# Kernel optimization log

Hardware: AMD Instinct MI355X
Metric: run time of the kernel (lower is better)

Reference implementation:

```python
import jax, jax.numpy as jnp
import numpy as np

B, R, A, V, L = 256, 512, 196, 10000, 2
I = R  # input_size == rnn_size (required for stacked layers)


def setup_inputs() -> dict:
    key = jax.random.key(0)
    ks = jax.random.split(key, 18)
    s = 0.05
    return {
        "x": jax.random.normal(ks[0], (B, I), jnp.float32),
        "att": jax.random.normal(ks[1], (B, A, R), jnp.float32),
        "inputs": jax.random.normal(ks[2], (2 * L, B, R), jnp.float32),
        "Wa2a": jax.random.normal(ks[3], (A, R), jnp.float32) * s,
        "ba2a": jnp.zeros((A,), jnp.float32),
        "Wh2a": jax.random.normal(ks[4], (A, R), jnp.float32) * s,
        "bh2a": jnp.zeros((A,), jnp.float32),
        "wd2d": jax.random.normal(ks[5], (A,), jnp.float32) * s,
        "bd2d": jnp.zeros((1,), jnp.float32),
        "Wi2h": jax.random.normal(ks[6], (4 * R, I), jnp.float32) * s,
        "bi2h": jnp.zeros((4 * R,), jnp.float32),
        "Wh2h": jax.random.normal(ks[7], (4 * R, R), jnp.float32) * s,
        "bh2h": jnp.zeros((4 * R,), jnp.float32),
        "Wr2a": jax.random.normal(ks[8], (4 * R, R), jnp.float32) * s,
        "br2a": jnp.zeros((4 * R,), jnp.float32),
        "Wproj": jax.random.normal(ks[9], (V, R), jnp.float32) * s,
        "bproj": jnp.zeros((V,), jnp.float32),
    }


def reference(x, att, inputs, Wa2a, ba2a, Wh2a, bh2a, wd2d, bd2d,
              Wi2h, bi2h, Wh2h, bh2h, Wr2a, br2a, Wproj, bproj):
    # att: [B, A, R]  (A spatial positions, R features); inputs: [2L, B, R]
    states = []
    cur = x
    # a2a(att) is layer-independent but the original recomputes it; einsum below
    # is cheap so we keep the per-layer structure faithful & simple.
    for i in range(L):
        prev_c = inputs[2 * i]
        prev_h = inputs[2 * i + 1]
        # attention scoring: att_v[b,i,a] + att_h[b,i] (unsqueeze(2).expand)
        att_v = jnp.einsum('bir,ar->bia', att, Wa2a) + ba2a          # [B,A,A]
        att_h = prev_h @ Wh2a.T + bh2a                               # [B,A]
        dot = jnp.tanh(att_v + att_h[:, :, None])                    # [B,A,A]
        score = jnp.einsum('bia,a->bi', dot, wd2d) + bd2d            # [B,A]
        w = jax.nn.softmax(score, axis=-1)                           # [B,A]
        att_res = jnp.einsum('bir,bi->br', att, w)                   # [B,R]
        sums = (cur @ Wi2h.T + bi2h) + (prev_h @ Wh2h.T + bh2h) + (att_res @ Wr2a.T + br2a)
        gates = jax.nn.sigmoid(sums[:, :3 * R])
        in_gate = gates[:, :R]
        forget_gate = gates[:, R:2 * R]
        out_gate = gates[:, 2 * R:3 * R]
        in_transform = jnp.tanh(sums[:, 3 * R:])
        next_c = forget_gate * prev_c + in_gate * in_transform
        next_h = out_gate * jnp.tanh(next_c)
        states.append(next_c)
        states.append(next_h)
        cur = next_h
    logsoft = jax.nn.log_softmax(cur @ Wproj.T + bproj, axis=-1)     # [B,V]
    return jnp.stack(states), logsoft
```

## Files before the change

### kernel.cpp

```cpp
#include <hip/hip_runtime.h>
#include <hip/hip_bf16.h>
#include <cstdint>
#include <cstddef>

#define BB 256
#define RR 512
#define AA 196
#define VV 10000
#define MATT (BB*AA)
#define NT13 13

typedef float f32x4 __attribute__((ext_vector_type(4)));
typedef __bf16 bf16x8 __attribute__((ext_vector_type(8)));
typedef __bf16 bf16x4 __attribute__((ext_vector_type(4)));

#define MFMA16(a,b,c) __builtin_amdgcn_mfma_f32_16x16x32_bf16(a,b,c,0,0,0)

__device__ __forceinline__ float fast_tanh(float x){
  float ax = fabsf(x);
  float e = __expf(-2.0f*ax);
  float t = __fdividef(1.0f - e, 1.0f + e);
  return x < 0.0f ? -t : t;
}

__device__ __forceinline__ void gload16(const void* gsrc, void* ldsdst){
  __builtin_amdgcn_global_load_lds(
      (const __attribute__((address_space(1))) unsigned int*)gsrc,
      (__attribute__((address_space(3))) unsigned int*)ldsdst,
      16, 0, 0);
}

#define ABAR   asm volatile("s_barrier" ::: "memory")
#define WVM(N) asm volatile("s_waitcnt vmcnt(" #N ")" ::: "memory")

#define CVT8(a, f0, f1) do { \
  a[0]=(__bf16)(f0).x; a[1]=(__bf16)(f0).y; a[2]=(__bf16)(f0).z; a[3]=(__bf16)(f0).w; \
  a[4]=(__bf16)(f1).x; a[5]=(__bf16)(f1).y; a[6]=(__bf16)(f1).z; a[7]=(__bf16)(f1).w; \
} while(0)

__global__ void cvt4_k(const float* __restrict__ src, __bf16* __restrict__ dst, int n4){
  int i = blockIdx.x*256 + threadIdx.x;
  if (i < n4){
    float4 v = ((const float4*)src)[i];
    bf16x4 o;
    o[0]=(__bf16)v.x; o[1]=(__bf16)v.y; o[2]=(__bf16)v.z; o[3]=(__bf16)v.w;
    ((bf16x4*)dst)[i] = o;
  }
}

__global__ void cvt_padrows_k(const float* __restrict__ src, __bf16* __restrict__ dst, int nvalid){
  int i = blockIdx.x*256 + threadIdx.x;
  int row = i >> 9;
  dst[i] = (__bf16)((row < nvalid) ? src[(size_t)row*512 + (i & 511)] : 0.0f);
}

__global__ void wcat2_k(const float* __restrict__ Wi2h, const float* __restrict__ Wh2h,
                        const float* __restrict__ Wr2a, __bf16* __restrict__ Wcat){
  int k = blockIdx.x*256 + threadIdx.x;
  int n = blockIdx.y;
  float v;
  if (k < 512)       v = Wi2h[n*512 + k];
  else if (k < 1024) v = Wh2h[n*512 + (k-512)];
  else               v = Wr2a[n*512 + (k-1024)];
  Wcat[(size_t)n*1536 + k] = (__bf16)v;
}

__global__ void build_small_k(const float* __restrict__ ba2a, const float* __restrict__ wd2d,
                              const float* __restrict__ bi2h, const float* __restrict__ bh2h,
                              const float* __restrict__ br2a,
                              float* __restrict__ ba_pad, float* __restrict__ wd_pad,
                              float* __restrict__ bcat){
  int i = blockIdx.x*256 + threadIdx.x;
  if (i < 2048){
    bcat[i] = bi2h[i] + bh2h[i] + br2a[i];
  } else if (i < 2048+208){
    int j = i - 2048; ba_pad[j] = (j < AA) ? ba2a[j] : 0.0f;
  } else if (i < 2048+416){
    int j = i - 2256; wd_pad[j] = (j < AA) ? wd2d[j] : 0.0f;
  }
}

__global__ __launch_bounds__(256,4) void gemm3_k(
    const __bf16* __restrict__ A, const __bf16* __restrict__ Bw,
    const float* __restrict__ bias, float* __restrict__ C,
    int N, int K, int NC)
{
  __shared__ __bf16 AshAll[3*2048];
  __shared__ __bf16 BshAll[3*4096];
  const int t = threadIdx.x;
  const int l = t & 63;
  const int w = t >> 6;
  const int l15 = l & 15;
  const int g  = l >> 4;
  const int rho = l15 & 7;
  const int mrow = blockIdx.y*32;
  const int ncb  = blockIdx.x*64;

  const int arow = t >> 3, aj = t & 7;
  const __bf16* as_ = A + (size_t)(mrow + arow)*K + ((aj ^ (arow&7)) << 3);
  const int aoff = w*512;
  const __bf16* bs0_ = Bw + (size_t)(ncb + arow)*K      + ((aj ^ (arow&7)) << 3);
  const __bf16* bs1_ = Bw + (size_t)(ncb + 32 + arow)*K + ((aj ^ (arow&7)) << 3);
  const int boff0 = w*512;
  const int boff1 = 2048 + w*512;

#define G3_STAGE(B, CH) do { \
    gload16(as_  + (CH)*64, AshAll + (B)*2048 + aoff); \
    gload16(bs0_ + (CH)*64, BshAll + (B)*4096 + boff0); \
    gload16(bs1_ + (CH)*64, BshAll + (B)*4096 + boff1); \
  } while(0)

  f32x4 acc0 = {}, acc1 = {};

#define G3_COMPUTE(B) do { \
    const __bf16* As_ = AshAll + (B)*2048; \
    const __bf16* Bs_ = BshAll + (B)*4096; \
    _Pragma("unroll") \
    for (int s_ = 0; s_ < 2; s_++){ \
      int q_ = (((s_<<2)+g) ^ rho) << 3; \
      bf16x8 a0_ = *(const bf16x8*)(As_ + l15*64 + q_); \
      bf16x8 a1_ = *(const bf16x8*)(As_ + (l15+16)*64 + q_); \
      bf16x8 b_  = *(const bf16x8*)(Bs_ + (w*16+l15)*64 + q_); \
      acc0 = MFMA16(a0_, b_, acc0); \
      acc1 = MFMA16(a1_, b_, acc1); \
    } \
  } while(0)

  G3_STAGE(0,0); G3_STAGE(1,1); G3_STAGE(2,2);
  WVM(6); ABAR;
  int buf = 0;
  for (int c = 0; c < NC; c++){
    G3_COMPUTE(buf);
    if (c + 3 < NC){
      ABAR;
      G3_STAGE(buf, c+3);
      WVM(6); ABAR;
    } else if (c == NC-3){
      WVM(3); ABAR;
    } else if (c == NC-2){
      WVM(0); ABAR;
    }
    buf = (buf == 2) ? 0 : buf + 1;
  }

  int col = ncb + w*16 + l15;
  if (col < N){
    float bv = bias[col];
    #pragma unroll
    for (int r = 0; r < 4; r++){
      C[(size_t)(mrow + g*4 + r)*N + col]      = acc0[r] + bv;
      C[(size_t)(mrow + 16 + g*4 + r)*N + col] = acc1[r] + bv;
    }
  }
#undef G3_STAGE
#undef G3_COMPUTE
}

__global__ __launch_bounds__(256,2) void att_score5_k(
    const float* __restrict__ att, const __bf16* __restrict__ Wa2a_p,
    const float* __restrict__ ba_pad, const float* __restrict__ wd_pad,
    const float* __restrict__ att_h, float* __restrict__ score)
{
  __shared__ __bf16 Bsh[3*13312];
  const int t = threadIdx.x;
  const int l = t & 63;
  const int w = t >> 6;
  const int l15 = l & 15;
  const int g  = l >> 4;
  const int rho = l15 & 7;
  const int rowbase = blockIdx.x * 64;

  const __bf16* bsrc[7]; int bslot[7];
  #pragma unroll
  for (int i = 0; i < 7; i++){
    int id = i*4 + w;
    if (id >= 26) id -= 2;
    int slotbase = id*64;
    int slot = slotbase + l;
    int row = slot >> 3;
    int j   = slot & 7;
    bslot[i] = slotbase*8;
    bsrc[i]  = Wa2a_p + (size_t)row*RR + ((j ^ (row&7))<<3);
  }

  const float* pa = att + (size_t)(rowbase + w*16 + l15)*RR + g*8;

  f32x4 acc[NT13] = {};
  float4 p00,p01,p02,p03, p10,p11,p12,p13, p20,p21,p22,p23;

#define SC_STAGE(B, KC) do { \
    _Pragma("unroll") \
    for (int i_ = 0; i_ < 7; i_++) gload16(bsrc[i_] + (KC), Bsh + (B)*13312 + bslot[i_]); \
  } while(0)
#define SC_LOADA(S, KC) do { \
    p##S##0 = *(const float4*)(pa + (KC)); \
    p##S##1 = *(const float4*)(pa + (KC) + 4); \
    p##S##2 = *(const float4*)(pa + (KC) + 32); \
    p##S##3 = *(const float4*)(pa + (KC) + 36); \
  } while(0)
#define SC_COMPUTE(B, S) do { \
    { bf16x8 a_; CVT8(a_, p##S##0, p##S##1); \
      const int sw_ = (g ^ rho) << 3; \
      _Pragma("unroll") \
      for (int nt_ = 0; nt_ < NT13; nt_++){ \
        bf16x8 b_ = *(const bf16x8*)&Bsh[(B)*13312 + nt_*1024 + l15*64 + sw_]; \
        acc[nt_] = MFMA16(a_, b_, acc[nt_]); } } \
    { bf16x8 a_; CVT8(a_, p##S##2, p##S##3); \
      const int sw_ = ((4 + g) ^ rho) << 3; \
      _Pragma("unroll") \
      for (int nt_ = 0; nt_ < NT13; nt_++){ \
        bf16x8 b_ = *(const bf16x8*)&Bsh[(B)*13312 + nt_*1024 + l15*64 + sw_]; \
        acc[nt_] = MFMA16(a_, b_, acc[nt_]); } } \
  } while(0)

  SC_STAGE(0,0);   SC_LOADA(0,0);
  SC_STAGE(1,64);  SC_LOADA(1,64);
  SC_STAGE(2,128); SC_LOADA(2,128);
  WVM(22); ABAR;
  SC_COMPUTE(0,0); ABAR; SC_STAGE(0,192); SC_LOADA(0,192); WVM(22); ABAR;
  SC_COMPUTE(1,1); ABAR; SC_STAGE(1,256); SC_LOADA(1,256); WVM(22); ABAR;
  SC_COMPUTE(2,2); ABAR; SC_STAGE(2,320); SC_LOADA(2,320); WVM(22); ABAR;
  SC_COMPUTE(0,0); ABAR; SC_STAGE(0,384); SC_LOADA(0,384); WVM(22); ABAR;
  SC_COMPUTE(1,1); ABAR; SC_STAGE(1,448); SC_LOADA(1,448); WVM(22); ABAR;
  SC_COMPUTE(2,2); WVM(11); ABAR;
  SC_COMPUTE(0,0); WVM(0);  ABAR;
  SC_COMPUTE(1,1);

  float wdv[NT13], bav[NT13];
  #pragma unroll
  for (int nt = 0; nt < NT13; nt++){
    int col = nt*16 + l15;
    wdv[nt] = wd_pad[col];
    bav[nt] = ba_pad[col];
  }
  #pragma unroll
  for (int r = 0; r < 4; r++){
    int row = rowbase + w*16 + g*4 + r;
    float ah0 = att_h[row];
    float ah1 = att_h[MATT + row];
    float s0 = 0.0f, s1 = 0.0f;
    #pragma unroll
    for (int nt = 0; nt < NT13; nt++){
      float v = acc[nt][r] + bav[nt];
      s0 += fast_tanh(v + ah0) * wdv[nt];
      s1 += fast_tanh(v + ah1) * wdv[nt];
    }
    #pragma unroll
    for (int o = 1; o < 16; o <<= 1){
      s0 += __shfl_xor(s0, o, 16);
      s1 += __shfl_xor(s1, o, 16);
    }
    if (l15 == 0){
      score[row] = s0;
      score[MATT + row] = s1;
    }
  }
#undef SC_STAGE
#undef SC_LOADA
#undef SC_COMPUTE
}

__global__ void softmax196_k(const float* __restrict__ score, float* __restrict__ wsm){
  int lb = blockIdx.x;
  int t = threadIdx.x;
  const float* s = score + (size_t)lb*AA;
  float v0 = (t      < AA) ? s[t]       : -3.4e38f;
  float v1 = (t+64   < AA) ? s[t+64]    : -3.4e38f;
  float v2 = (t+128  < AA) ? s[t+128]   : -3.4e38f;
  float v3 = (t+192  < AA) ? s[t+192]   : -3.4e38f;
  float mx = fmaxf(fmaxf(v0,v1), fmaxf(v2,v3));
  #pragma unroll
  for (int o = 1; o < 64; o <<= 1) mx = fmaxf(mx, __shfl_xor(mx, o, 64));
  float e0 = (t      < AA) ? __expf(v0 - mx) : 0.0f;
  float e1 = (t+64   < AA) ? __expf(v1 - mx) : 0.0f;
  float e2 = (t+128  < AA) ? __expf(v2 - mx) : 0.0f;
  float e3 = (t+192  < AA) ? __expf(v3 - mx) : 0.0f;
  float sum = e0+e1+e2+e3;
  #pragma unroll
  for (int o = 1; o < 64; o <<= 1) sum += __shfl_xor(sum, o, 64);
  float inv = 1.0f / sum;
  float* o_ = wsm + (size_t)lb*AA;
  if (t      < AA) o_[t]     = e0*inv;
  if (t+64   < AA) o_[t+64]  = e1*inv;
  if (t+128  < AA) o_[t+128] = e2*inv;
  if (t+192  < AA) o_[t+192] = e3*inv;
}

__global__ __launch_bounds__(512) void attres3_k(
    const float* __restrict__ att, const float* __restrict__ wsm,
    const float* __restrict__ x, const float* __restrict__ inputs,
    __bf16* __restrict__ Xcat0, __bf16* __restrict__ Xcat1){
  int b = blockIdx.x, t = threadIdx.x;
  __shared__ float w0[208], w1[208];
  __shared__ float4 redv[4][128];
  if (t < AA) w0[t] = wsm[(size_t)b*AA + t];
  int t2 = t - 256;
  if (t2 >= 0 && t2 < AA) w1[t2] = wsm[(size_t)(256+b)*AA + t2];
  Xcat0[(size_t)b*1536 + t]       = (__bf16)x[(size_t)b*512 + t];
  Xcat0[(size_t)b*1536 + 512 + t] = (__bf16)inputs[(size_t)1*131072 + b*512 + t];
  Xcat1[(size_t)b*1536 + 512 + t] = (__bf16)inputs[(size_t)3*131072 + b*512 + t];
  __syncthreads();
  int cg = t & 127, ig = t >> 7;
  const float4* ap = (const float4*)(att + (size_t)b*AA*RR) + cg;
  float4 s0 = {0,0,0,0}, s1 = {0,0,0,0};
  #pragma unroll 4
  for (int i = ig; i < AA; i += 4){
    float4 v = ap[(size_t)i*128];
    float a0 = w0[i], a1 = w1[i];
    s0.x += v.x*a0; s0.y += v.y*a0; s0.z += v.z*a0; s0.w += v.w*a0;
    s1.x += v.x*a1; s1.y += v.y*a1; s1.z += v.z*a1; s1.w += v.w*a1;
  }
  redv[ig][cg] = s0; __syncthreads();
  if (t < 128){
    float4 a = redv[0][t], b4 = redv[1][t], c4 = redv[2][t], d4 = redv[3][t];
    __bf16* o = Xcat0 + (size_t)b*1536 + 1024 + t*4;
    o[0]=(__bf16)(a.x+b4.x+c4.x+d4.x); o[1]=(__bf16)(a.y+b4.y+c4.y+d4.y);
    o[2]=(__bf16)(a.z+b4.z+c4.z+d4.z); o[3]=(__bf16)(a.w+b4.w+c4.w+d4.w);
  }
  __syncthreads();
  redv[ig][cg] = s1; __syncthreads();
  if (t < 128){
    float4 a = redv[0][t], b4 = redv[1][t], c4 = redv[2][t], d4 = redv[3][t];
    __bf16* o = Xcat1 + (size_t)b*1536 + 1024 + t*4;
    o[0]=(__bf16)(a.x+b4.x+c4.x+d4.x); o[1]=(__bf16)(a.y+b4.y+c4.y+d4.y);
    o[2]=(__bf16)(a.z+b4.z+c4.z+d4.z); o[3]=(__bf16)(a.w+b4.w+c4.w+d4.w);
  }
}

__global__ void gate_k(const float* __restrict__ sums, const float* __restrict__ prev_c,
                       float* __restrict__ out_c, float* __restrict__ out_h,
                       __bf16* __restrict__ hdst, int hstride){
  int idx = blockIdx.x*256 + threadIdx.x;
  int b = idx >> 9, r = idx & 511;
  const float* s = sums + (size_t)b*2048;
  float ig = 1.0f/(1.0f + __expf(-s[r]));
  float fg = 1.0f/(1.0f + __expf(-s[512+r]));
  float og = 1.0f/(1.0f + __expf(-s[1024+r]));
  float g  = fast_tanh(s[1536+r]);
  float c = fg*prev_c[idx] + ig*g;
  float h = og*fast_tanh(c);
  out_c[idx] = c;
  out_h[idx] = h;
  hdst[(size_t)b*hstride + r] = (__bf16)h;
}

__global__ void logsoftmax_k(const float* __restrict__ logits, float* __restrict__ out){
  int b = blockIdx.x, t = threadIdx.x;
  __shared__ float red[4], red2[4];
  const float* p = logits + (size_t)b*VV;
  float mx = -3.4e38f;
  for (int i = t; i < VV; i += 256) mx = fmaxf(mx, p[i]);
  #pragma unroll
  for (int o = 1; o < 64; o <<= 1) mx = fmaxf(mx, __shfl_xor(mx, o, 64));
  if ((t & 63) == 0) red[t >> 6] = mx;
  __syncthreads();
  mx = fmaxf(fmaxf(red[0], red[1]), fmaxf(red[2], red[3]));
  float sum = 0.0f;
  for (int i = t; i < VV; i += 256) sum += __expf(p[i] - mx);
  #pragma unroll
  for (int o = 1; o < 64; o <<= 1) sum += __shfl_xor(sum, o, 64);
  if ((t & 63) == 0) red2[t >> 6] = sum;
  __syncthreads();
  sum = red2[0] + red2[1] + red2[2] + red2[3];
  float lse = mx + logf(sum);
  float* q = out + (size_t)b*VV;
  for (int i = t; i < VV; i += 256) q[i] = p[i] - lse;
}

extern "C" void kernel_launch(void* const* d_in, const int* in_sizes, int n_in,
                              void* d_out_, int out_size, void* d_ws, size_t ws_size,
                              hipStream_t stream){
  const float* x     = (const float*)d_in[0];
  const float* att   = (const float*)d_in[1];
  const float* inputs= (const float*)d_in[2];
  const float* Wa2a  = (const float*)d_in[3];
  const float* ba2a  = (const float*)d_in[4];
  const float* Wh2a  = (const float*)d_in[5];
  const float* bh2a  = (const float*)d_in[6];
  const float* wd2d  = (const float*)d_in[7];
  const float* Wi2h  = (const float*)d_in[9];
  const float* bi2h  = (const float*)d_in[10];
  const float* Wh2h  = (const float*)d_in[11];
  const float* bh2h  = (const float*)d_in[12];
  const float* Wr2a  = (const float*)d_in[13];
  const float* br2a  = (const float*)d_in[14];
  const float* Wproj = (const float*)d_in[15];
  const float* bproj = (const float*)d_in[16];
  float* d_out = (float*)d_out_;

  char* wsp = (char*)d_ws;
  auto alloc = [&](size_t bytes)->char*{
    char* p = wsp;
    wsp += (bytes + 255) & ~(size_t)255;
    return p;
  };
  __bf16* Wa2a_p   = (__bf16*)alloc((size_t)208*RR*2);
  __bf16* Wh2a_pad = (__bf16*)alloc((size_t)256*RR*2);
  __bf16* Wcat_bf  = (__bf16*)alloc((size_t)2048*1536*2);
  __bf16* Wproj_bf = (__bf16*)alloc((size_t)10048*RR*2);
  __bf16* inp_bf   = (__bf16*)alloc((size_t)512*RR*2);
  float* ba_pad = (float*)alloc(208*4);
  float* wd_pad = (float*)alloc(208*4);
  float* bcat   = (float*)alloc(2048*4);
  float* att_h  = (float*)alloc((size_t)2*MATT*4);
  float* score  = (float*)alloc((size_t)2*MATT*4);
  float* wsm    = (float*)alloc((size_t)2*MATT*4);
  __bf16* Xcat0 = (__bf16*)alloc((size_t)BB*1536*2);
  __bf16* Xcat1 = (__bf16*)alloc((size_t)BB*1536*2);
  float* sums   = (float*)alloc((size_t)BB*2048*4);
  __bf16* h1_bf = (__bf16*)alloc((size_t)BB*RR*2);
  float* logits = (float*)alloc((size_t)BB*VV*4);

  cvt_padrows_k<<<(208*512)/256, 256, 0, stream>>>(Wa2a, Wa2a_p, AA);
  cvt_padrows_k<<<(256*512)/256, 256, 0, stream>>>(Wh2a, Wh2a_pad, AA);
  cvt_padrows_k<<<(10048*512)/256, 256, 0, stream>>>(Wproj, Wproj_bf, VV);
  cvt4_k<<<(131072/4)/256, 256, 0, stream>>>(inputs + 1*131072, inp_bf, 131072/4);
  cvt4_k<<<(131072/4)/256, 256, 0, stream>>>(inputs + 3*131072, inp_bf + 131072, 131072/4);
  wcat2_k<<<dim3(6,2048), 256, 0, stream>>>(Wi2h, Wh2h, Wr2a, Wcat_bf);
  build_small_k<<<10, 256, 0, stream>>>(ba2a, wd2d, bi2h, bh2h, br2a, ba_pad, wd_pad, bcat);

  gemm3_k<<<dim3(4,16), 256, 0, stream>>>(inp_bf, Wh2a_pad, bh2a, att_h, AA, 512, 8);
  att_score5_k<<<784, 256, 0, stream>>>(att, Wa2a_p, ba_pad, wd_pad, att_h, score);
  softmax196_k<<<512, 64, 0, stream>>>(score, wsm);
  attres3_k<<<256, 512, 0, stream>>>(att, wsm, x, inputs, Xcat0, Xcat1);

  gemm3_k<<<dim3(32,8), 256, 0, stream>>>(Xcat0, Wcat_bf, bcat, sums, 2048, 1536, 24);
  gate_k<<<512, 256, 0, stream>>>(sums, inputs, d_out, d_out + 131072, Xcat1, 1536);
  gemm3_k<<<dim3(32,8), 256, 0, stream>>>(Xcat1, Wcat_bf, bcat, sums, 2048, 1536, 24);
  gate_k<<<512, 256, 0, stream>>>(sums, inputs + 2*131072, d_out + 2*131072, d_out + 3*131072, h1_bf, 512);

  gemm3_k<<<dim3(157,8), 256, 0, stream>>>(h1_bf, Wproj_bf, bproj, logits, VV, 512, 8);
  logsoftmax_k<<<256, 256, 0, stream>>>(logits, d_out + 4*131072);
}
```

Baseline: 166.5 us.

## Pre-convert att to bf16 and retile attention scoring with split N halves

Adds a pass that converts the full att tensor to bf16 once. The attention-score kernel is restructured to stage both att and Wa2a tiles into LDS via async loads, using 128-row by 128-column tiles over a 2D grid, and writes partial scores per column half. The softmax then sums the two halves, and the att-weighted reduction reads the bf16 att copy. The intent is to reduce per-block register and LDS pressure, raise occupancy and halve att read traffic in later kernels. The cost is an extra conversion pass over about 100 MB of fp32 att, plus padding the A dimension to 256, which does wasted MFMA work on the padded columns.

```diff
diff --git a/kernel.cpp b/kernel.cpp
--- a/kernel.cpp
+++ b/kernel.cpp
@@ -8,7 +8,7 @@
 #define AA 196
 #define VV 10000
 #define MATT (BB*AA)
-#define NT13 13
+#define NT8 8
 
 typedef float f32x4 __attribute__((ext_vector_type(4)));
 typedef __bf16 bf16x8 __attribute__((ext_vector_type(8)));
@@ -32,11 +32,6 @@
 
 #define ABAR   asm volatile("s_barrier" ::: "memory")
 #define WVM(N) asm volatile("s_waitcnt vmcnt(" #N ")" ::: "memory")
-
-#define CVT8(a, f0, f1) do { \
-  a[0]=(__bf16)(f0).x; a[1]=(__bf16)(f0).y; a[2]=(__bf16)(f0).z; a[3]=(__bf16)(f0).w; \
-  a[4]=(__bf16)(f1).x; a[5]=(__bf16)(f1).y; a[6]=(__bf16)(f1).z; a[7]=(__bf16)(f1).w; \
-} while(0)
 
 __global__ void cvt4_k(const float* __restrict__ src, __bf16* __restrict__ dst, int n4){
   int i = blockIdx.x*256 + threadIdx.x;
@@ -73,10 +68,10 @@
   int i = blockIdx.x*256 + threadIdx.x;
   if (i < 2048){
     bcat[i] = bi2h[i] + bh2h[i] + br2a[i];
-  } else if (i < 2048+208){
+  } else if (i < 2048+256){
     int j = i - 2048; ba_pad[j] = (j < AA) ? ba2a[j] : 0.0f;
-  } else if (i < 2048+416){
-    int j = i - 2256; wd_pad[j] = (j < AA) ? wd2d[j] : 0.0f;
+  } else if (i < 2048+512){
+    int j = i - 2304; wd_pad[j] = (j < AA) ? wd2d[j] : 0.0f;
   }
 }
 
@@ -156,118 +151,121 @@
 #undef G3_COMPUTE
 }
 
-__global__ __launch_bounds__(256,2) void att_score5_k(
-    const float* __restrict__ att, const __bf16* __restrict__ Wa2a_p,
+__global__ __launch_bounds__(256,3) void att_score6_k(
+    const __bf16* __restrict__ att_bf, const __bf16* __restrict__ Wa2a_p,
     const float* __restrict__ ba_pad, const float* __restrict__ wd_pad,
-    const float* __restrict__ att_h, float* __restrict__ score)
+    const float* __restrict__ att_h, float* __restrict__ sp)
 {
-  __shared__ __bf16 Bsh[3*13312];
+  __shared__ __bf16 Ash[3*4096];
+  __shared__ __bf16 Bsh[3*4096];
   const int t = threadIdx.x;
   const int l = t & 63;
   const int w = t >> 6;
   const int l15 = l & 15;
   const int g  = l >> 4;
-  const int rho = l15 & 7;
-  const int rowbase = blockIdx.x * 64;
-
-  const __bf16* bsrc[7]; int bslot[7];
-  #pragma unroll
-  for (int i = 0; i < 7; i++){
+  const int rowbase = blockIdx.x * 128;
+  const int half = blockIdx.y;
+
+  const __bf16* asrc[2]; const __bf16* bsrc[2]; int slotb[2];
+  #pragma unroll
+  for (int i = 0; i < 2; i++){
     int id = i*4 + w;
-    if (id >= 26) id -= 2;
-    int slotbase = id*64;
-    int slot = slotbase + l;
-    int row = slot >> 3;
-    int j   = slot & 7;
-    bslot[i] = slotbase*8;
-    bsrc[i]  = Wa2a_p + (size_t)row*RR + ((j ^ (row&7))<<3);
-  }
-
-  const float* pa = att + (size_t)(rowbase + w*16 + l15)*RR + g*8;
-
-  f32x4 acc[NT13] = {};
-  float4 p00,p01,p02,p03, p10,p11,p12,p13, p20,p21,p22,p23;
-
-#define SC_STAGE(B, KC) do { \
+    int slot = id*64 + l;
+    int row = slot >> 2, j = slot & 3;
+    int jj = j ^ ((row>>1)&3);
+    slotb[i] = id*512;
+    asrc[i] = att_bf + (size_t)(rowbase + row)*RR + (jj<<3);
+    bsrc[i] = Wa2a_p + (size_t)(half*128 + row)*RR + (jj<<3);
+  }
+
+  f32x4 acc0[NT8] = {}; f32x4 acc1[NT8] = {};
+
+#define S6_STAGE(BC, KC) do { \
+    gload16(asrc[0] + (KC), Ash + (BC)*4096 + slotb[0]); \
+    gload16(asrc[1] + (KC), Ash + (BC)*4096 + slotb[1]); \
+    gload16(bsrc[0] + (KC), Bsh + (BC)*4096 + slotb[0]); \
+    gload16(bsrc[1] + (KC), Bsh + (BC)*4096 + slotb[1]); \
+  } while(0)
+
+  const int r0 = w*32 + l15, r1 = r0 + 16;
+  const int ao0 = r0*32 + ((g ^ ((r0>>1)&3))<<3);
+  const int ao1 = r1*32 + ((g ^ ((r1>>1)&3))<<3);
+
+#define S6_COMPUTE(BC) do { \
+    const __bf16* As_ = Ash + (BC)*4096; \
+    const __bf16* Bs_ = Bsh + (BC)*4096; \
+    bf16x8 a0_ = *(const bf16x8*)(As_ + ao0); \
+    bf16x8 a1_ = *(const bf16x8*)(As_ + ao1); \
     _Pragma("unroll") \
-    for (int i_ = 0; i_ < 7; i_++) gload16(bsrc[i_] + (KC), Bsh + (B)*13312 + bslot[i_]); \
+    for (int nt_ = 0; nt_ < NT8; nt_++){ \
+      int br_ = nt_*16 + l15; \
+      bf16x8 b_ = *(const bf16x8*)(Bs_ + br_*32 + ((g ^ ((br_>>1)&3))<<3)); \
+      acc0[nt_] = MFMA16(a0_, b_, acc0[nt_]); \
+      acc1[nt_] = MFMA16(a1_, b_, acc1[nt_]); \
+    } \
   } while(0)
-#define SC_LOADA(S, KC) do { \
-    p##S##0 = *(const float4*)(pa + (KC)); \
-    p##S##1 = *(const float4*)(pa + (KC) + 4); \
-    p##S##2 = *(const float4*)(pa + (KC) + 32); \
-    p##S##3 = *(const float4*)(pa + (KC) + 36); \
-  } while(0)
-#define SC_COMPUTE(B, S) do { \
-    { bf16x8 a_; CVT8(a_, p##S##0, p##S##1); \
-      const int sw_ = (g ^ rho) << 3; \
-      _Pragma("unroll") \
-      for (int nt_ = 0; nt_ < NT13; nt_++){ \
-        bf16x8 b_ = *(const bf16x8*)&Bsh[(B)*13312 + nt_*1024 + l15*64 + sw_]; \
-        acc[nt_] = MFMA16(a_, b_, acc[nt_]); } } \
-    { bf16x8 a_; CVT8(a_, p##S##2, p##S##3); \
-      const int sw_ = ((4 + g) ^ rho) << 3; \
-      _Pragma("unroll") \
-      for (int nt_ = 0; nt_ < NT13; nt_++){ \
-        bf16x8 b_ = *(const bf16x8*)&Bsh[(B)*13312 + nt_*1024 + l15*64 + sw_]; \
-        acc[nt_] = MFMA16(a_, b_, acc[nt_]); } } \
-  } while(0)
-
-  SC_STAGE(0,0);   SC_LOADA(0,0);
-  SC_STAGE(1,64);  SC_LOADA(1,64);
-  SC_STAGE(2,128); SC_LOADA(2,128);
-  WVM(22); ABAR;
-  SC_COMPUTE(0,0); ABAR; SC_STAGE(0,192); SC_LOADA(0,192); WVM(22); ABAR;
-  SC_COMPUTE(1,1); ABAR; SC_STAGE(1,256); SC_LOADA(1,256); WVM(22); ABAR;
-  SC_COMPUTE(2,2); ABAR; SC_STAGE(2,320); SC_LOADA(2,320); WVM(22); ABAR;
-  SC_COMPUTE(0,0); ABAR; SC_STAGE(0,384); SC_LOADA(0,384); WVM(22); ABAR;
-  SC_COMPUTE(1,1); ABAR; SC_STAGE(1,448); SC_LOADA(1,448); WVM(22); ABAR;
-  SC_COMPUTE(2,2); WVM(11); ABAR;
-  SC_COMPUTE(0,0); WVM(0);  ABAR;
-  SC_COMPUTE(1,1);
-
-  float wdv[NT13], bav[NT13];
-  #pragma unroll
-  for (int nt = 0; nt < NT13; nt++){
-    int col = nt*16 + l15;
+
+  S6_STAGE(0,0); S6_STAGE(1,32); S6_STAGE(2,64);
+  WVM(8); ABAR;
+  #pragma unroll
+  for (int c = 0; c < 16; c++){
+    S6_COMPUTE(c%3);
+    if (c < 13){
+      ABAR;
+      S6_STAGE(c%3, (c+3)*32);
+      WVM(8); ABAR;
+    } else if (c == 13){
+      WVM(4); ABAR;
+    } else if (c == 14){
+      WVM(0); ABAR;
+    }
+  }
+
+  float wdv[NT8], bav[NT8];
+  #pragma unroll
+  for (int nt = 0; nt < NT8; nt++){
+    int col = half*128 + nt*16 + l15;
     wdv[nt] = wd_pad[col];
     bav[nt] = ba_pad[col];
   }
   #pragma unroll
-  for (int r = 0; r < 4; r++){
-    int row = rowbase + w*16 + g*4 + r;
-    float ah0 = att_h[row];
-    float ah1 = att_h[MATT + row];
-    float s0 = 0.0f, s1 = 0.0f;
+  for (int mt = 0; mt < 2; mt++){
     #pragma unroll
-    for (int nt = 0; nt < NT13; nt++){
-      float v = acc[nt][r] + bav[nt];
-      s0 += fast_tanh(v + ah0) * wdv[nt];
-      s1 += fast_tanh(v + ah1) * wdv[nt];
+    for (int r = 0; r < 4; r++){
+      int row = rowbase + w*32 + mt*16 + g*4 + r;
+      float ah0 = att_h[row];
+      float ah1 = att_h[MATT + row];
+      float s0 = 0.0f, s1 = 0.0f;
+      #pragma unroll
+      for (int nt = 0; nt < NT8; nt++){
+        float v = (mt ? acc1[nt][r] : acc0[nt][r]) + bav[nt];
+        s0 += fast_tanh(v + ah0) * wdv[nt];
+        s1 += fast_tanh(v + ah1) * wdv[nt];
+      }
+      #pragma unroll
+      for (int o = 1; o < 16; o <<= 1){
+        s0 += __shfl_xor(s0, o, 16);
+        s1 += __shfl_xor(s1, o, 16);
+      }
+      if (l15 == 0){
+        sp[(size_t)half*2*MATT + row]        = s0;
+        sp[(size_t)half*2*MATT + MATT + row] = s1;
+      }
     }
-    #pragma unroll
-    for (int o = 1; o < 16; o <<= 1){
-      s0 += __shfl_xor(s0, o, 16);
-      s1 += __shfl_xor(s1, o, 16);
-    }
-    if (l15 == 0){
-      score[row] = s0;
-      score[MATT + row] = s1;
-    }
-  }
-#undef SC_STAGE
-#undef SC_LOADA
-#undef SC_COMPUTE
-}
-
-__global__ void softmax196_k(const float* __restrict__ score, float* __restrict__ wsm){
+  }
+#undef S6_STAGE
+#undef S6_COMPUTE
+}
+
+__global__ void softmax196b_k(const float* __restrict__ sp, float* __restrict__ wsm){
   int lb = blockIdx.x;
   int t = threadIdx.x;
-  const float* s = score + (size_t)lb*AA;
-  float v0 = (t      < AA) ? s[t]       : -3.4e38f;
-  float v1 = (t+64   < AA) ? s[t+64]    : -3.4e38f;
-  float v2 = (t+128  < AA) ? s[t+128]   : -3.4e38f;
-  float v3 = (t+192  < AA) ? s[t+192]   : -3.4e38f;
+  const float* p = sp + (size_t)(lb>>8)*MATT + (size_t)(lb&255)*AA;
+  const float* q = p + (size_t)2*MATT;
+  float v0 = (t      < AA) ? p[t]     + q[t]     : -3.4e38f;
+  float v1 = (t+64   < AA) ? p[t+64]  + q[t+64]  : -3.4e38f;
+  float v2 = (t+128  < AA) ? p[t+128] + q[t+128] : -3.4e38f;
+  float v3 = (t+192  < AA) ? p[t+192] + q[t+192] : -3.4e38f;
   float mx = fmaxf(fmaxf(v0,v1), fmaxf(v2,v3));
   #pragma unroll
   for (int o = 1; o < 64; o <<= 1) mx = fmaxf(mx, __shfl_xor(mx, o, 64));
@@ -286,13 +284,13 @@
   if (t+192  < AA) o_[t+192] = e3*inv;
 }
 
-__global__ __launch_bounds__(512) void attres3_k(
-    const float* __restrict__ att, const float* __restrict__ wsm,
+__global__ __launch_bounds__(512) void attres4_k(
+    const __bf16* __restrict__ att_bf, const float* __restrict__ wsm,
     const float* __restrict__ x, const float* __restrict__ inputs,
     __bf16* __restrict__ Xcat0, __bf16* __restrict__ Xcat1){
   int b = blockIdx.x, t = threadIdx.x;
-  __shared__ float w0[208], w1[208];
-  __shared__ float4 redv[4][128];
+  __shared__ float w0[AA+4], w1[AA+4];
+  __shared__ float red[8][520];
   if (t < AA) w0[t] = wsm[(size_t)b*AA + t];
   int t2 = t - 256;
   if (t2 >= 0 && t2 < AA) w1[t2] = wsm[(size_t)(256+b)*AA + t2];
@@ -300,30 +298,36 @@
   Xcat0[(size_t)b*1536 + 512 + t] = (__bf16)inputs[(size_t)1*131072 + b*512 + t];
   Xcat1[(size_t)b*1536 + 512 + t] = (__bf16)inputs[(size_t)3*131072 + b*512 + t];
   __syncthreads();
-  int cg = t & 127, ig = t >> 7;
-  const float4* ap = (const float4*)(att + (size_t)b*AA*RR) + cg;
-  float4 s0 = {0,0,0,0}, s1 = {0,0,0,0};
-  #pragma unroll 4
-  for (int i = ig; i < AA; i += 4){
-    float4 v = ap[(size_t)i*128];
+  int cg = t & 63, ig = t >> 6;
+  const __bf16* ap = att_bf + (size_t)b*AA*RR + cg*8;
+  float s0[8] = {}, s1[8] = {};
+  for (int i = ig; i < AA; i += 8){
+    bf16x8 v = *(const bf16x8*)(ap + (size_t)i*RR);
     float a0 = w0[i], a1 = w1[i];
-    s0.x += v.x*a0; s0.y += v.y*a0; s0.z += v.z*a0; s0.w += v.w*a0;
-    s1.x += v.x*a1; s1.y += v.y*a1; s1.z += v.z*a1; s1.w += v.w*a1;
-  }
-  redv[ig][cg] = s0; __syncthreads();
-  if (t < 128){
-    float4 a = redv[0][t], b4 = redv[1][t], c4 = redv[2][t], d4 = redv[3][t];
-    __bf16* o = Xcat0 + (size_t)b*1536 + 1024 + t*4;
-    o[0]=(__bf16)(a.x+b4.x+c4.x+d4.x); o[1]=(__bf16)(a.y+b4.y+c4.y+d4.y);
-    o[2]=(__bf16)(a.z+b4.z+c4.z+d4.z); o[3]=(__bf16)(a.w+b4.w+c4.w+d4.w);
-  }
-  __syncthreads();
-  redv[ig][cg] = s1; __syncthreads();
-  if (t < 128){
-    float4 a = redv[0][t], b4 = redv[1][t], c4 = redv[2][t], d4 = redv[3][t];
-    __bf16* o = Xcat1 + (size_t)b*1536 + 1024 + t*4;
-    o[0]=(__bf16)(a.x+b4.x+c4.x+d4.x); o[1]=(__bf16)(a.y+b4.y+c4.y+d4.y);
-    o[2]=(__bf16)(a.z+b4.z+c4.z+d4.z); o[3]=(__bf16)(a.w+b4.w+c4.w+d4.w);
+    #pragma unroll
+    for (int e = 0; e < 8; e++){
+      float f = (float)v[e];
+      s0[e] += f*a0; s1[e] += f*a1;
+    }
+  }
+  #pragma unroll
+  for (int e = 0; e < 8; e++) red[ig][cg*8+e] = s0[e];
+  __syncthreads();
+  {
+    float a = 0;
+    #pragma unroll
+    for (int q = 0; q < 8; q++) a += red[q][t];
+    Xcat0[(size_t)b*1536 + 1024 + t] = (__bf16)a;
+  }
+  __syncthreads();
+  #pragma unroll
+  for (int e = 0; e < 8; e++) red[ig][cg*8+e] = s1[e];
+  __syncthreads();
+  {
+    float a = 0;
+    #pragma unroll
+    for (int q = 0; q < 8; q++) a += red[q][t];
+    Xcat1[(size_t)b*1536 + 1024 + t] = (__bf16)a;
   }
 }
 
@@ -394,16 +398,17 @@
     wsp += (bytes + 255) & ~(size_t)255;
     return p;
   };
-  __bf16* Wa2a_p   = (__bf16*)alloc((size_t)208*RR*2);
+  __bf16* att_bf   = (__bf16*)alloc((size_t)MATT*RR*2);
+  __bf16* Wa2a_p   = (__bf16*)alloc((size_t)256*RR*2);
   __bf16* Wh2a_pad = (__bf16*)alloc((size_t)256*RR*2);
   __bf16* Wcat_bf  = (__bf16*)alloc((size_t)2048*1536*2);
   __bf16* Wproj_bf = (__bf16*)alloc((size_t)10048*RR*2);
   __bf16* inp_bf   = (__bf16*)alloc((size_t)512*RR*2);
-  float* ba_pad = (float*)alloc(208*4);
-  float* wd_pad = (float*)alloc(208*4);
+  float* ba_pad = (float*)alloc(256*4);
+  float* wd_pad = (float*)alloc(256*4);
   float* bcat   = (float*)alloc(2048*4);
   float* att_h  = (float*)alloc((size_t)2*MATT*4);
-  float* score  = (float*)alloc((size_t)2*MATT*4);
+  float* sp     = (float*)alloc((size_t)4*MATT*4);
   float* wsm    = (float*)alloc((size_t)2*MATT*4);
   __bf16* Xcat0 = (__bf16*)alloc((size_t)BB*1536*2);
   __bf16* Xcat1 = (__bf16*)alloc((size_t)BB*1536*2);
@@ -411,7 +416,8 @@
   __bf16* h1_bf = (__bf16*)alloc((size_t)BB*RR*2);
   float* logits = (float*)alloc((size_t)BB*VV*4);
 
-  cvt_padrows_k<<<(208*512)/256, 256, 0, stream>>>(Wa2a, Wa2a_p, AA);
+  cvt4_k<<<(MATT*RR/4)/256, 256, 0, stream>>>(att, att_bf, MATT*RR/4);
+  cvt_padrows_k<<<(256*512)/256, 256, 0, stream>>>(Wa2a, Wa2a_p, AA);
   cvt_padrows_k<<<(256*512)/256, 256, 0, stream>>>(Wh2a, Wh2a_pad, AA);
   cvt_padrows_k<<<(10048*512)/256, 256, 0, stream>>>(Wproj, Wproj_bf, VV);
   cvt4_k<<<(131072/4)/256, 256, 0, stream>>>(inputs + 1*131072, inp_bf, 131072/4);
@@ -420,9 +426,9 @@
   build_small_k<<<10, 256, 0, stream>>>(ba2a, wd2d, bi2h, bh2h, br2a, ba_pad, wd_pad, bcat);
 
   gemm3_k<<<dim3(4,16), 256, 0, stream>>>(inp_bf, Wh2a_pad, bh2a, att_h, AA, 512, 8);
-  att_score5_k<<<784, 256, 0, stream>>>(att, Wa2a_p, ba_pad, wd_pad, att_h, score);
-  softmax196_k<<<512, 64, 0, stream>>>(score, wsm);
-  attres3_k<<<256, 512, 0, stream>>>(att, wsm, x, inputs, Xcat0, Xcat1);
+  att_score6_k<<<dim3(392,2), 256, 0, stream>>>(att_bf, Wa2a_p, ba_pad, wd_pad, att_h, sp);
+  softmax196b_k<<<512, 64, 0, stream>>>(sp, wsm);
+  attres4_k<<<256, 512, 0, stream>>>(att_bf, wsm, x, inputs, Xcat0, Xcat1);
 
   gemm3_k<<<dim3(32,8), 256, 0, stream>>>(Xcat0, Wcat_bf, bcat, sums, 2048, 1536, 24);
   gate_k<<<512, 256, 0, stream>>>(sums, inputs, d_out, d_out + 131072, Xcat1, 1536);
```

New measurement: 181.5 us. 9.0% more time.

## Fuse attention scoring, softmax and weighted sum into one per-batch kernel

Applied to the files above, without the earlier changes.

Replaces the three kernels for attention scoring (MFMA GEMM plus tanh dot), softmax and attention-weighted sum with a single kernel that runs one block per batch row. Each block computes its 196x196 (padded to 256) score tile through LDS double-buffering, reduces and softmaxes in shared memory, then re-reads att for the weighted sum. This removes the score and softmax-weight global round trips and two launches. In exchange the grid drops to 256 blocks, padding wastes MFMA work, and att is read twice within the block (the second read may hit cache).

```diff
diff --git a/kernel.cpp b/kernel.cpp
--- a/kernel.cpp
+++ b/kernel.cpp
@@ -8,7 +8,6 @@
 #define AA 196
 #define VV 10000
 #define MATT (BB*AA)
-#define NT13 13
 
 typedef float f32x4 __attribute__((ext_vector_type(4)));
 typedef __bf16 bf16x8 __attribute__((ext_vector_type(8)));
@@ -73,10 +72,10 @@
   int i = blockIdx.x*256 + threadIdx.x;
   if (i < 2048){
     bcat[i] = bi2h[i] + bh2h[i] + br2a[i];
-  } else if (i < 2048+208){
+  } else if (i < 2048+256){
     int j = i - 2048; ba_pad[j] = (j < AA) ? ba2a[j] : 0.0f;
-  } else if (i < 2048+416){
-    int j = i - 2256; wd_pad[j] = (j < AA) ? wd2d[j] : 0.0f;
+  } else if (i < 2048+512){
+    int j = i - 2304; wd_pad[j] = (j < AA) ? wd2d[j] : 0.0f;
   }
 }
 
@@ -156,175 +155,183 @@
 #undef G3_COMPUTE
 }
 
-__global__ __launch_bounds__(256,2) void att_score5_k(
+__global__ __launch_bounds__(512,2) void attfull_k(
     const float* __restrict__ att, const __bf16* __restrict__ Wa2a_p,
     const float* __restrict__ ba_pad, const float* __restrict__ wd_pad,
-    const float* __restrict__ att_h, float* __restrict__ score)
+    const float* __restrict__ att_h, const float* __restrict__ x,
+    const float* __restrict__ inputs,
+    __bf16* __restrict__ Xcat0, __bf16* __restrict__ Xcat1)
 {
-  __shared__ __bf16 Bsh[3*13312];
+  __shared__ char smem[67584];
   const int t = threadIdx.x;
+  const int b = blockIdx.x;
   const int l = t & 63;
   const int w = t >> 6;
-  const int l15 = l & 15;
-  const int g  = l >> 4;
-  const int rho = l15 & 7;
-  const int rowbase = blockIdx.x * 64;
-
-  const __bf16* bsrc[7]; int bslot[7];
-  #pragma unroll
-  for (int i = 0; i < 7; i++){
-    int id = i*4 + w;
-    if (id >= 26) id -= 2;
-    int slotbase = id*64;
-    int slot = slotbase + l;
-    int row = slot >> 3;
-    int j   = slot & 7;
-    bslot[i] = slotbase*8;
-    bsrc[i]  = Wa2a_p + (size_t)row*RR + ((j ^ (row&7))<<3);
-  }
-
-  const float* pa = att + (size_t)(rowbase + w*16 + l15)*RR + g*8;
-
-  f32x4 acc[NT13] = {};
-  float4 p00,p01,p02,p03, p10,p11,p12,p13, p20,p21,p22,p23;
-
-#define SC_STAGE(B, KC) do { \
-    _Pragma("unroll") \
-    for (int i_ = 0; i_ < 7; i_++) gload16(bsrc[i_] + (KC), Bsh + (B)*13312 + bslot[i_]); \
-  } while(0)
-#define SC_LOADA(S, KC) do { \
-    p##S##0 = *(const float4*)(pa + (KC)); \
-    p##S##1 = *(const float4*)(pa + (KC) + 4); \
-    p##S##2 = *(const float4*)(pa + (KC) + 32); \
-    p##S##3 = *(const float4*)(pa + (KC) + 36); \
-  } while(0)
-#define SC_COMPUTE(B, S) do { \
-    { bf16x8 a_; CVT8(a_, p##S##0, p##S##1); \
-      const int sw_ = (g ^ rho) << 3; \
-      _Pragma("unroll") \
-      for (int nt_ = 0; nt_ < NT13; nt_++){ \
-        bf16x8 b_ = *(const bf16x8*)&Bsh[(B)*13312 + nt_*1024 + l15*64 + sw_]; \
-        acc[nt_] = MFMA16(a_, b_, acc[nt_]); } } \
-    { bf16x8 a_; CVT8(a_, p##S##2, p##S##3); \
-      const int sw_ = ((4 + g) ^ rho) << 3; \
-      _Pragma("unroll") \
-      for (int nt_ = 0; nt_ < NT13; nt_++){ \
-        bf16x8 b_ = *(const bf16x8*)&Bsh[(B)*13312 + nt_*1024 + l15*64 + sw_]; \
-        acc[nt_] = MFMA16(a_, b_, acc[nt_]); } } \
-  } while(0)
-
-  SC_STAGE(0,0);   SC_LOADA(0,0);
-  SC_STAGE(1,64);  SC_LOADA(1,64);
-  SC_STAGE(2,128); SC_LOADA(2,128);
-  WVM(22); ABAR;
-  SC_COMPUTE(0,0); ABAR; SC_STAGE(0,192); SC_LOADA(0,192); WVM(22); ABAR;
-  SC_COMPUTE(1,1); ABAR; SC_STAGE(1,256); SC_LOADA(1,256); WVM(22); ABAR;
-  SC_COMPUTE(2,2); ABAR; SC_STAGE(2,320); SC_LOADA(2,320); WVM(22); ABAR;
-  SC_COMPUTE(0,0); ABAR; SC_STAGE(0,384); SC_LOADA(0,384); WVM(22); ABAR;
-  SC_COMPUTE(1,1); ABAR; SC_STAGE(1,448); SC_LOADA(1,448); WVM(22); ABAR;
-  SC_COMPUTE(2,2); WVM(11); ABAR;
-  SC_COMPUTE(0,0); WVM(0);  ABAR;
-  SC_COMPUTE(1,1);
-
-  float wdv[NT13], bav[NT13];
-  #pragma unroll
-  for (int nt = 0; nt < NT13; nt++){
-    int col = nt*16 + l15;
-    wdv[nt] = wd_pad[col];
-    bav[nt] = ba_pad[col];
-  }
-  #pragma unroll
-  for (int r = 0; r < 4; r++){
-    int row = rowbase + w*16 + g*4 + r;
-    float ah0 = att_h[row];
-    float ah1 = att_h[MATT + row];
-    float s0 = 0.0f, s1 = 0.0f;
-    #pragma unroll
-    for (int nt = 0; nt < NT13; nt++){
-      float v = acc[nt][r] + bav[nt];
-      s0 += fast_tanh(v + ah0) * wdv[nt];
-      s1 += fast_tanh(v + ah1) * wdv[nt];
-    }
-    #pragma unroll
-    for (int o = 1; o < 16; o <<= 1){
-      s0 += __shfl_xor(s0, o, 16);
-      s1 += __shfl_xor(s1, o, 16);
-    }
-    if (l15 == 0){
-      score[row] = s0;
-      score[MATT + row] = s1;
-    }
-  }
-#undef SC_STAGE
-#undef SC_LOADA
-#undef SC_COMPUTE
-}
-
-__global__ void softmax196_k(const float* __restrict__ score, float* __restrict__ wsm){
-  int lb = blockIdx.x;
-  int t = threadIdx.x;
-  const float* s = score + (size_t)lb*AA;
-  float v0 = (t      < AA) ? s[t]       : -3.4e38f;
-  float v1 = (t+64   < AA) ? s[t+64]    : -3.4e38f;
-  float v2 = (t+128  < AA) ? s[t+128]   : -3.4e38f;
-  float v3 = (t+192  < AA) ? s[t+192]   : -3.4e38f;
-  float mx = fmaxf(fmaxf(v0,v1), fmaxf(v2,v3));
-  #pragma unroll
-  for (int o = 1; o < 64; o <<= 1) mx = fmaxf(mx, __shfl_xor(mx, o, 64));
-  float e0 = (t      < AA) ? __expf(v0 - mx) : 0.0f;
-  float e1 = (t+64   < AA) ? __expf(v1 - mx) : 0.0f;
-  float e2 = (t+128  < AA) ? __expf(v2 - mx) : 0.0f;
-  float e3 = (t+192  < AA) ? __expf(v3 - mx) : 0.0f;
-  float sum = e0+e1+e2+e3;
-  #pragma unroll
-  for (int o = 1; o < 64; o <<= 1) sum += __shfl_xor(sum, o, 64);
-  float inv = 1.0f / sum;
-  float* o_ = wsm + (size_t)lb*AA;
-  if (t      < AA) o_[t]     = e0*inv;
-  if (t+64   < AA) o_[t+64]  = e1*inv;
-  if (t+128  < AA) o_[t+128] = e2*inv;
-  if (t+192  < AA) o_[t+192] = e3*inv;
-}
-
-__global__ __launch_bounds__(512) void attres3_k(
-    const float* __restrict__ att, const float* __restrict__ wsm,
-    const float* __restrict__ x, const float* __restrict__ inputs,
-    __bf16* __restrict__ Xcat0, __bf16* __restrict__ Xcat1){
-  int b = blockIdx.x, t = threadIdx.x;
-  __shared__ float w0[208], w1[208];
-  __shared__ float4 redv[4][128];
-  if (t < AA) w0[t] = wsm[(size_t)b*AA + t];
-  int t2 = t - 256;
-  if (t2 >= 0 && t2 < AA) w1[t2] = wsm[(size_t)(256+b)*AA + t2];
+  const int wr = w >> 2, wc = w & 3;
+  const int l15 = l & 15, g = l >> 4;
+
   Xcat0[(size_t)b*1536 + t]       = (__bf16)x[(size_t)b*512 + t];
   Xcat0[(size_t)b*1536 + 512 + t] = (__bf16)inputs[(size_t)1*131072 + b*512 + t];
   Xcat1[(size_t)b*1536 + 512 + t] = (__bf16)inputs[(size_t)3*131072 + b*512 + t];
-  __syncthreads();
-  int cg = t & 127, ig = t >> 7;
-  const float4* ap = (const float4*)(att + (size_t)b*AA*RR) + cg;
+  float* ahsh = (float*)(smem + 65536);
+  { int li = t >> 8, i = t & 255;
+    ahsh[li*256 + i] = (i < AA) ? att_h[((size_t)li*256 + b)*AA + i] : 0.0f; }
+
+  const int sr = t >> 1, sh = t & 1;
+  const float*  aSrc = att + ((size_t)b*AA + (sr < AA ? sr : AA-1))*RR + sh*16;
+  const __bf16* bSrc = Wa2a_p + (size_t)sr*RR + sh*16;
+  const int rb = sr*64;
+  const int q0 = (((sh*2)   ^ (sr&3))<<4);
+  const int q1 = (((sh*2+1) ^ (sr&3))<<4);
+
+  f32x4 acc[8][4] = {};
+  float4 af0, af1, af2, af3;
+  uint4  bq0, bq1;
+
+  const int aswz  = (g ^ (l15&3)) << 4;
+  const int abase = (wr*128 + l15)*64 + aswz;
+  const int bbase = (wc*64  + l15)*64 + aswz;
+
+#define AF_LOADP(KC) do { \
+    af0 = *(const float4*)(aSrc + (KC));      af1 = *(const float4*)(aSrc + (KC) + 4); \
+    af2 = *(const float4*)(aSrc + (KC) + 8);  af3 = *(const float4*)(aSrc + (KC) + 12); \
+    bq0 = *(const uint4*)(bSrc + (KC));       bq1 = *(const uint4*)(bSrc + (KC) + 8); \
+  } while(0)
+
+#define STAGE_WR(BUF) do { \
+    char* Ab = smem + (BUF)*16384; \
+    char* Bb = smem + 32768 + (BUF)*16384; \
+    bf16x8 w0_, w1_; CVT8(w0_, af0, af1); CVT8(w1_, af2, af3); \
+    *(bf16x8*)(Ab + rb + q0) = w0_; \
+    *(bf16x8*)(Ab + rb + q1) = w1_; \
+    *(uint4*)(Bb + rb + q0) = bq0; \
+    *(uint4*)(Bb + rb + q1) = bq1; \
+  } while(0)
+
+#define K_COMPUTE(BUF) do { \
+    const char* Ab = smem + (BUF)*16384; \
+    const char* Bb = smem + 32768 + (BUF)*16384; \
+    bf16x8 bfr[4]; \
+    _Pragma("unroll") \
+    for (int ct = 0; ct < 4; ct++) bfr[ct] = *(const bf16x8*)(Bb + bbase + ct*1024); \
+    _Pragma("unroll") \
+    for (int rt = 0; rt < 8; rt++){ \
+      bf16x8 afr = *(const bf16x8*)(Ab + abase + rt*1024); \
+      _Pragma("unroll") \
+      for (int ct = 0; ct < 4; ct++) acc[rt][ct] = MFMA16(afr, bfr[ct], acc[rt][ct]); \
+    } \
+  } while(0)
+
+  AF_LOADP(0);
+  STAGE_WR(0);
+  AF_LOADP(32);
+  __syncthreads();
+  #pragma unroll
+  for (int c = 0; c < 16; c++){
+    K_COMPUTE(c & 1);
+    if (c < 15) STAGE_WR((c+1) & 1);
+    if (c < 14) AF_LOADP((c+2)*32);
+    __syncthreads();
+  }
+
+  float bav[4], wdv[4];
+  #pragma unroll
+  for (int ct = 0; ct < 4; ct++){
+    int col = wc*64 + ct*16 + l15;
+    bav[ct] = ba_pad[col];
+    wdv[ct] = wd_pad[col];
+  }
+  float* spart = (float*)smem;
+  #pragma unroll
+  for (int rt = 0; rt < 8; rt++){
+    #pragma unroll
+    for (int rg = 0; rg < 4; rg++){
+      int row = wr*128 + rt*16 + g*4 + rg;
+      float ah0 = ahsh[row];
+      float ah1 = ahsh[256 + row];
+      float s0 = 0.0f, s1 = 0.0f;
+      #pragma unroll
+      for (int ct = 0; ct < 4; ct++){
+        float v = acc[rt][ct][rg] + bav[ct];
+        s0 += fast_tanh(v + ah0) * wdv[ct];
+        s1 += fast_tanh(v + ah1) * wdv[ct];
+      }
+      #pragma unroll
+      for (int o = 1; o < 16; o <<= 1){
+        s0 += __shfl_xor(s0, o, 16);
+        s1 += __shfl_xor(s1, o, 16);
+      }
+      if (l15 == 0 && row < AA){
+        spart[(0*4 + wc)*256 + row] = s0;
+        spart[(1*4 + wc)*256 + row] = s1;
+      }
+    }
+  }
+  __syncthreads();
+
+  float* wv = (float*)(smem + 10240);
+  if (w < 2){
+    const float* sl = spart + w*4*256;
+    float v0_[4]; float e_[4];
+    #pragma unroll
+    for (int j = 0; j < 4; j++){
+      int i = l + j*64;
+      float s = sl[i] + sl[256+i] + sl[512+i] + sl[768+i];
+      v0_[j] = (i < AA) ? s : -3.4e38f;
+    }
+    float mx = fmaxf(fmaxf(v0_[0],v0_[1]), fmaxf(v0_[2],v0_[3]));
+    #pragma unroll
+    for (int o = 1; o < 64; o <<= 1) mx = fmaxf(mx, __shfl_xor(mx, o, 64));
+    float sum = 0.0f;
+    #pragma unroll
+    for (int j = 0; j < 4; j++){
+      int i = l + j*64;
+      e_[j] = (i < AA) ? __expf(v0_[j] - mx) : 0.0f;
+      sum += e_[j];
+    }
+    #pragma unroll
+    for (int o = 1; o < 64; o <<= 1) sum += __shfl_xor(sum, o, 64);
+    float inv = 1.0f / sum;
+    #pragma unroll
+    for (int j = 0; j < 4; j++){
+      int i = l + j*64;
+      if (i < AA) wv[w*256 + i] = e_[j]*inv;
+    }
+  }
+  __syncthreads();
+
+  int r4 = t & 127, ig = t >> 7;
+  const float4* ap = (const float4*)(att + (size_t)b*AA*RR) + r4;
   float4 s0 = {0,0,0,0}, s1 = {0,0,0,0};
-  #pragma unroll 4
   for (int i = ig; i < AA; i += 4){
     float4 v = ap[(size_t)i*128];
-    float a0 = w0[i], a1 = w1[i];
-    s0.x += v.x*a0; s0.y += v.y*a0; s0.z += v.z*a0; s0.w += v.w*a0;
-    s1.x += v.x*a1; s1.y += v.y*a1; s1.z += v.z*a1; s1.w += v.w*a1;
-  }
-  redv[ig][cg] = s0; __syncthreads();
+    float w0_ = wv[i], w1_ = wv[256+i];
+    s0.x += v.x*w0_; s0.y += v.y*w0_; s0.z += v.z*w0_; s0.w += v.w*w0_;
+    s1.x += v.x*w1_; s1.y += v.y*w1_; s1.z += v.z*w1_; s1.w += v.w*w1_;
+  }
+  float4* redv = (float4*)smem;
+  redv[ig*128 + r4] = s0;
+  __syncthreads();
   if (t < 128){
-    float4 a = redv[0][t], b4 = redv[1][t], c4 = redv[2][t], d4 = redv[3][t];
-    __bf16* o = Xcat0 + (size_t)b*1536 + 1024 + t*4;
+    float4 a = redv[t], b4 = redv[128+t], c4 = redv[256+t], d4 = redv[384+t];
+    bf16x4 o;
     o[0]=(__bf16)(a.x+b4.x+c4.x+d4.x); o[1]=(__bf16)(a.y+b4.y+c4.y+d4.y);
     o[2]=(__bf16)(a.z+b4.z+c4.z+d4.z); o[3]=(__bf16)(a.w+b4.w+c4.w+d4.w);
-  }
-  __syncthreads();
-  redv[ig][cg] = s1; __syncthreads();
+    *(bf16x4*)(Xcat0 + (size_t)b*1536 + 1024 + t*4) = o;
+  }
+  __syncthreads();
+  redv[ig*128 + r4] = s1;
+  __syncthreads();
   if (t < 128){
-    float4 a = redv[0][t], b4 = redv[1][t], c4 = redv[2][t], d4 = redv[3][t];
-    __bf16* o = Xcat1 + (size_t)b*1536 + 1024 + t*4;
+    float4 a = redv[t], b4 = redv[128+t], c4 = redv[256+t], d4 = redv[384+t];
+    bf16x4 o;
     o[0]=(__bf16)(a.x+b4.x+c4.x+d4.x); o[1]=(__bf16)(a.y+b4.y+c4.y+d4.y);
     o[2]=(__bf16)(a.z+b4.z+c4.z+d4.z); o[3]=(__bf16)(a.w+b4.w+c4.w+d4.w);
-  }
+    *(bf16x4*)(Xcat1 + (size_t)b*1536 + 1024 + t*4) = o;
+  }
+#undef AF_LOADP
+#undef STAGE_WR
+#undef K_COMPUTE
 }
 
 __global__ void gate_k(const float* __restrict__ sums, const float* __restrict__ prev_c,
@@ -394,24 +401,22 @@
     wsp += (bytes + 255) & ~(size_t)255;
     return p;
   };
-  __bf16* Wa2a_p   = (__bf16*)alloc((size_t)208*RR*2);
+  __bf16* Wa2a_p   = (__bf16*)alloc((size_t)256*RR*2);
   __bf16* Wh2a_pad = (__bf16*)alloc((size_t)256*RR*2);
   __bf16* Wcat_bf  = (__bf16*)alloc((size_t)2048*1536*2);
   __bf16* Wproj_bf = (__bf16*)alloc((size_t)10048*RR*2);
   __bf16* inp_bf   = (__bf16*)alloc((size_t)512*RR*2);
-  float* ba_pad = (float*)alloc(208*4);
-  float* wd_pad = (float*)alloc(208*4);
+  float* ba_pad = (float*)alloc(256*4);
+  float* wd_pad = (float*)alloc(256*4);
   float* bcat   = (float*)alloc(2048*4);
   float* att_h  = (float*)alloc((size_t)2*MATT*4);
-  float* score  = (float*)alloc((size_t)2*MATT*4);
-  float* wsm    = (float*)alloc((size_t)2*MATT*4);
   __bf16* Xcat0 = (__bf16*)alloc((size_t)BB*1536*2);
   __bf16* Xcat1 = (__bf16*)alloc((size_t)BB*1536*2);
   float* sums   = (float*)alloc((size_t)BB*2048*4);
   __bf16* h1_bf = (__bf16*)alloc((size_t)BB*RR*2);
   float* logits = (float*)alloc((size_t)BB*VV*4);
 
-  cvt_padrows_k<<<(208*512)/256, 256, 0, stream>>>(Wa2a, Wa2a_p, AA);
+  cvt_padrows_k<<<(256*512)/256, 256, 0, stream>>>(Wa2a, Wa2a_p, AA);
   cvt_padrows_k<<<(256*512)/256, 256, 0, stream>>>(Wh2a, Wh2a_pad, AA);
   cvt_padrows_k<<<(10048*512)/256, 256, 0, stream>>>(Wproj, Wproj_bf, VV);
   cvt4_k<<<(131072/4)/256, 256, 0, stream>>>(inputs + 1*131072, inp_bf, 131072/4);
@@ -420,9 +425,8 @@
   build_small_k<<<10, 256, 0, stream>>>(ba2a, wd2d, bi2h, bh2h, br2a, ba_pad, wd_pad, bcat);
 
   gemm3_k<<<dim3(4,16), 256, 0, stream>>>(inp_bf, Wh2a_pad, bh2a, att_h, AA, 512, 8);
-  att_score5_k<<<784, 256, 0, stream>>>(att, Wa2a_p, ba_pad, wd_pad, att_h, score);
-  softmax196_k<<<512, 64, 0, stream>>>(score, wsm);
-  attres3_k<<<256, 512, 0, stream>>>(att, wsm, x, inputs, Xcat0, Xcat1);
+
+  attfull_k<<<256, 512, 0, stream>>>(att, Wa2a_p, ba_pad, wd_pad, att_h, x, inputs, Xcat0, Xcat1);
 
   gemm3_k<<<dim3(32,8), 256, 0, stream>>>(Xcat0, Wcat_bf, bcat, sums, 2048, 1536, 24);
   gate_k<<<512, 256, 0, stream>>>(sums, inputs, d_out, d_out + 131072, Xcat1, 1536);
```

After: 167.3 us. Within noise of the previous version (+0.5%).
